# Kernel optimization log

Measured on AMD Instinct MI355X. Metric: run time of the kernel, lower is better.

## Reference

```python
import jax, jax.numpy as jnp
import numpy as np

HEADS = 4
DIM_HEAD = 128
HIDDEN = HEADS * DIM_HEAD  # 512
DIM = 256
EMBED = 256


def mish(x):
    return x * jnp.tanh(jax.nn.softplus(x))


def setup_inputs() -> dict:
    key = jax.random.key(0)
    k = jax.random.split(key, 7)
    b, a, f, t = 64, 8, DIM, 256
    x = jax.random.normal(k[0], (b, a, f, t), dtype=jnp.float32)
    time = jax.random.normal(k[1], (b, a, EMBED), dtype=jnp.float32)
    # to_qkv: Conv2d(dim, 3*hidden, 1, bias=False) -> weight [3*hidden, dim]
    w_qkv = jax.random.normal(k[2], (3 * HIDDEN, DIM), dtype=jnp.float32) * (1.0 / np.sqrt(DIM))
    # time_mlp: Mish -> Linear(embed, 3*hidden)
    w_time = jax.random.normal(k[3], (3 * HIDDEN, EMBED), dtype=jnp.float32) * (1.0 / np.sqrt(EMBED))
    b_time = jax.random.normal(k[4], (3 * HIDDEN,), dtype=jnp.float32) * 0.01
    # to_out: Conv2d(hidden, dim, 1) with bias
    w_out = jax.random.normal(k[5], (DIM, HIDDEN), dtype=jnp.float32) * (1.0 / np.sqrt(HIDDEN))
    b_out = jax.random.normal(k[6], (DIM,), dtype=jnp.float32) * 0.01
    return {"x": x, "time": time, "w_qkv": w_qkv, "w_time": w_time,
            "b_time": b_time, "w_out": w_out, "b_out": b_out}


def reference(x, time, w_qkv, w_time, b_time, w_out, b_out):
    b, a, f, t = x.shape
    heads, c = HEADS, DIM_HEAD
    # x: b a f t -> b f a t (channels-first for 1x1 conv)
    xp = jnp.transpose(x, (0, 2, 1, 3))  # [b, f, a, t]
    # 1x1 conv == channel GEMM
    qkv = jnp.einsum('of,bfat->boat', w_qkv, xp)  # [b, 3*hidden, a, t]
    # time MLP: Mish -> Linear; bias broadcast over t
    temb = mish(time) @ w_time.T + b_time          # [b, a, 3*hidden]
    temb = jnp.transpose(temb, (0, 2, 1))[..., None]  # [b, 3*hidden, a, 1]
    qkv = qkv + temb
    # 'b (qkv heads c) h w -> qkv (b h) heads c w' with h=a, w=t
    qkv = qkv.reshape(b, 3, heads, c, a, t)
    qkv = jnp.transpose(qkv, (1, 0, 4, 2, 3, 5)).reshape(3, b * a, heads, c, t)
    q, k, v = qkv[0], qkv[1], qkv[2]  # each [(b a), heads, c, t]
    k = jax.nn.softmax(k, axis=-1)
    # linear attention: context over keys/values, then apply to q
    context = jnp.einsum('bhdn,bhen->bhde', k, v)   # [(b a), heads, c, c]
    out = jnp.einsum('bhde,bhdn->bhen', context, q)  # [(b a), heads, c, t]
    # '(b h) heads c w -> b (heads c) h w'
    out = out.reshape(b, a, heads * c, t)
    out = jnp.transpose(out, (0, 2, 1, 3))  # [b, hidden, a, t]
    out = jnp.einsum('of,bfat->boat', w_out, out) + b_out[None, :, None, None]
    # b f a t -> b a f t
    return jnp.transpose(out, (0, 2, 1, 3))
```

## Files before the change

### kernel.cpp

```cpp
#include <hip/hip_runtime.h>

typedef __bf16 bf16;
typedef __bf16 bf16x4 __attribute__((ext_vector_type(4)));
typedef __bf16 bf16x8 __attribute__((ext_vector_type(8)));
typedef float  f32x4  __attribute__((ext_vector_type(4)));

#define TT    256
#define FF    256
#define NS    512

#define TSTR  40
#define TSZ2  (128 * TSTR)

#define SCHED0 __builtin_amdgcn_sched_barrier(0)
#define BAR    __builtin_amdgcn_s_barrier()
#define WAITVM(N) asm volatile("s_waitcnt vmcnt(" #N ")" ::: "memory")
#define WAITLGKM0 asm volatile("s_waitcnt lgkmcnt(0)" ::: "memory")

static __device__ inline f32x4 mfma16(bf16x8 a, bf16x8 b, f32x4 c) {
    return __builtin_amdgcn_mfma_f32_16x16x32_bf16(a, b, c, 0, 0, 0);
}

typedef const __attribute__((address_space(1))) unsigned int* gp_t;
typedef __attribute__((address_space(3))) unsigned int* lp_t;
static __device__ inline void gll16(const bf16* g, bf16* l) {
    __builtin_amdgcn_global_load_lds((gp_t)g, (lp_t)l, 16, 0, 0);
}


static __device__ inline void stage128g(const bf16* __restrict__ g, int ld, bf16* __restrict__ l) {
    int lane = threadIdx.x & 63, wv = threadIdx.x >> 6;
    int r = lane >> 2;
    int c8 = ((lane & 3) ^ ((lane >> 3) & 3)) * 8;
#pragma unroll
    for (int i = 0; i < 2; i++) {
        int row0 = wv * 32 + i * 16;
        gll16(g + (size_t)(row0 + r) * ld + c8, l + row0 * 32);
    }
}
static __device__ inline void stage8(const bf16* __restrict__ g, int ld, bf16* __restrict__ l) {
    int lane = threadIdx.x & 63, wv = threadIdx.x >> 6;
    int r = lane >> 2;
    int c8 = ((lane & 3) ^ ((lane >> 3) & 3)) * 8;
    int row0 = wv * 16;
    gll16(g + (size_t)(row0 + r) * ld + c8, l + row0 * 32);
}
static __device__ inline bf16x8 fragld(const bf16* __restrict__ l, int row0) {
    int lane = threadIdx.x & 63;
    int r15 = lane & 15;
    int kg = (lane >> 4) ^ ((r15 >> 1) & 3);
    return *(const bf16x8*)(l + (row0 + r15) * 32 + kg * 8);
}
static __device__ inline bf16x8 fragld_s(const bf16* __restrict__ l, int row0, int stride) {
    int lane = threadIdx.x & 63;
    return *(const bf16x8*)(l + (row0 + (lane & 15)) * stride + (lane >> 4) * 8);
}

__global__ __launch_bounds__(256) void k_cvt(const float4* __restrict__ src, bf16* __restrict__ dst) {
    int i = blockIdx.x * 256 + threadIdx.x;
    float4 v = src[i];
    bf16x4 o;
    o[0] = (__bf16)v.x; o[1] = (__bf16)v.y; o[2] = (__bf16)v.z; o[3] = (__bf16)v.w;
    *(bf16x4*)(dst + (size_t)i * 4) = o;
}

__global__ __launch_bounds__(256) void k_mish(const float4* __restrict__ src, bf16* __restrict__ dst) {
    int i = blockIdx.x * 256 + threadIdx.x;
    float4 v = src[i];
    float in[4] = {v.x, v.y, v.z, v.w};
    bf16x4 o;
#pragma unroll
    for (int j = 0; j < 4; j++) {
        float sp = log1pf(__expf(in[j]));
        o[j] = (__bf16)(in[j] * tanhf(sp));
    }
    *(bf16x4*)(dst + (size_t)i * 4) = o;
}

__global__ __launch_bounds__(256) void k_xpose(const float* __restrict__ x, bf16* __restrict__ xT) {
    __shared__ float tile[64][65];
    int bid = blockIdx.x;
    int s  = bid >> 4;
    int f0 = ((bid >> 2) & 3) * 64;
    int t0 = (bid & 3) * 64;
    int tid = threadIdx.x;
    int rr = tid >> 4;
    int cc = (tid & 15) * 4;
    const float* xp = x + ((size_t)(s * FF + f0)) * TT + t0;
#pragma unroll
    for (int i = 0; i < 4; i++) {
        int r = i * 16 + rr;
        float4 v = *(const float4*)(xp + (size_t)r * TT + cc);
        tile[r][cc] = v.x; tile[r][cc + 1] = v.y; tile[r][cc + 2] = v.z; tile[r][cc + 3] = v.w;
    }
    __syncthreads();
    bf16* op = xT + ((size_t)(s * TT + t0)) * FF + f0;
#pragma unroll
    for (int i = 0; i < 4; i++) {
        int tr = i * 16 + rr;
        bf16x4 o;
        o[0] = (__bf16)tile[cc][tr];     o[1] = (__bf16)tile[cc + 1][tr];
        o[2] = (__bf16)tile[cc + 2][tr]; o[3] = (__bf16)tile[cc + 3][tr];
        *(bf16x4*)(op + (size_t)tr * FF + cc) = o;
    }
}

__global__ __launch_bounds__(256) void k_temb(const bf16* __restrict__ wt, const bf16* __restrict__ mish,
                                              const float* __restrict__ bt, float* __restrict__ tembT) {
    __shared__ bf16 lA[128 * 32];
    __shared__ bf16 lB[128 * 32];
    int o0 = blockIdx.x * 128, s0 = blockIdx.y * 128;
    int tid = threadIdx.x, wv = tid >> 6, lane = tid & 63, qd = lane >> 4, c = lane & 15;
    f32x4 acc[2][8] = {};
    for (int k0 = 0; k0 < 256; k0 += 32) {
        __syncthreads();
        stage128g(wt + (size_t)o0 * 256 + k0, 256, lA);
        stage128g(mish + (size_t)s0 * 256 + k0, 256, lB);
        __syncthreads();
        bf16x8 a0 = fragld(lA, wv * 32), a1 = fragld(lA, wv * 32 + 16);
#pragma unroll
        for (int nt = 0; nt < 8; nt++) {
            bf16x8 b = fragld(lB, nt * 16);
            acc[0][nt] = mfma16(a0, b, acc[0][nt]);
            acc[1][nt] = mfma16(a1, b, acc[1][nt]);
        }
    }
#pragma unroll
    for (int mt = 0; mt < 2; mt++)
#pragma unroll
        for (int nt = 0; nt < 8; nt++)
#pragma unroll
            for (int r = 0; r < 4; r++) {
                int o = o0 + wv * 32 + mt * 16 + qd * 4 + r;
                int s = s0 + nt * 16 + c;
                tembT[(size_t)o * 512 + s] = acc[mt][nt][r] + bt[o];
            }
}

#define LXF(i)  ((bf16*)(smem + (size_t)(i) * 8192))
#define LWAF(i) ((bf16*)(smem + 24576 + (size_t)(i) * 8192))
#define LWBF(i) ((bf16*)(smem + 49152 + (size_t)(i) * 8192))
__global__ __launch_bounds__(512) void k_fused(const bf16* __restrict__ wqkv, const bf16* __restrict__ xT,
                                               const float* __restrict__ tembT, bf16* __restrict__ midT) {
    __shared__ __align__(16) char smem[156160];
    float* ls  = (float*)(smem + 73728);
    bf16*  lk  = (bf16*)(smem + 74240);
    bf16*  lct = (bf16*)(smem + 74240);
    bf16*  lv  = (bf16*)(smem + 115200);
    bf16*  lq  = (bf16*)(smem + 115200);

    int b = blockIdx.x;
    int w = (b & 7) * (4 * NS / 8) + (b >> 3);
    int s = w >> 2, h = w & 3;
    int tid = threadIdx.x, wv = tid >> 6, lane = tid & 63, qd = lane >> 4, c = lane & 15;
    const bf16* xs = xT + (size_t)s * (TT * FF);
    const bf16* Wq = wqkv + (size_t)(h * 128) * 256;
    const bf16* Wk = wqkv + (size_t)(512 + h * 128) * 256;
    const bf16* Wv = wqkv + (size_t)(1024 + h * 128) * 256;

    if (tid < 128) ls[tid] = 0.f;

    f32x4 cacc[8] = {};

    float tbk[8], tbv[8];
#pragma unroll
    for (int nt = 0; nt < 8; nt++) {
        tbk[nt] = tembT[(size_t)(512 + h * 128 + nt * 16 + c) * 512 + s];
        tbv[nt] = tembT[(size_t)(1024 + h * 128 + nt * 16 + c) * 512 + s];
    }

    for (int th = 0; th < 2; th++) {
        f32x4 kacc[8] = {}, vacc[8] = {};
        const bf16* xh = xs + (size_t)th * 128 * 256;
        stage8(xh,      256, LXF(0)); stage8(Wk,      256, LWAF(0)); stage8(Wv,      256, LWBF(0)); SCHED0;
        stage8(xh + 32, 256, LXF(1)); stage8(Wk + 32, 256, LWAF(1)); stage8(Wv + 32, 256, LWBF(1)); SCHED0;
        stage8(xh + 64, 256, LXF(2)); stage8(Wk + 64, 256, LWAF(2)); stage8(Wv + 64, 256, LWBF(2)); SCHED0;
#pragma unroll
        for (int t = 0; t < 8; t++) {
            if (t == 7)      { WAITVM(0); }
            else if (t == 6) { WAITVM(3); }
            else             { WAITVM(6); }
            SCHED0; BAR; SCHED0;
            int tb = t % 3;
            bf16x8 a0 = fragld(LXF(tb), wv * 16);
#pragma unroll
            for (int nt = 0; nt < 8; nt++) {
                kacc[nt] = mfma16(a0, fragld(LWAF(tb), nt * 16), kacc[nt]);
                vacc[nt] = mfma16(a0, fragld(LWBF(tb), nt * 16), vacc[nt]);
            }
            SCHED0; BAR; SCHED0;
            if (t + 3 < 8) {
                stage8(xh + (t + 3) * 32, 256, LXF(tb));
                stage8(Wk + (t + 3) * 32, 256, LWAF(tb));
                stage8(Wv + (t + 3) * 32, 256, LWBF(tb));
            }
            SCHED0;
        }
        {
            int addr0 = (wv >> 1) * TSZ2 + (wv & 1) * 16 + qd * 4;
#pragma unroll
            for (int nt = 0; nt < 8; nt++) {
                bf16x4 ok, ov;
                float ps = 0.f;
#pragma unroll
                for (int r = 0; r < 4; r++) {
                    bf16 e = (__bf16)__expf(kacc[nt][r] + tbk[nt]);
                    ok[r] = e; ps += (float)e;
                    ov[r] = (__bf16)(vacc[nt][r] + tbv[nt]);
                }
                int ad = addr0 + (nt * 16 + c) * TSTR;
                *(bf16x4*)(lk + ad) = ok;
                *(bf16x4*)(lv + ad) = ov;
                ps += __shfl_xor(ps, 16);
                ps += __shfl_xor(ps, 32);
                if (qd == 0) atomicAdd(&ls[nt * 16 + c], ps);
            }
        }
        __syncthreads();
#pragma unroll
        for (int tc = 0; tc < 4; tc++) {
            bf16x8 a0 = fragld_s(lv + tc * TSZ2, wv * 16, TSTR);
#pragma unroll
            for (int nt = 0; nt < 8; nt++)
                cacc[nt] = mfma16(a0, fragld_s(lk + tc * TSZ2, nt * 16, TSTR), cacc[nt]);
        }
        __syncthreads();
    }

    stage8(xs,      256, LXF(0)); stage8(Wq,      256, LWAF(0)); SCHED0;
    stage8(xs + 32, 256, LXF(1)); stage8(Wq + 32, 256, LWAF(1)); SCHED0;
    stage8(xs + 64, 256, LXF(2)); stage8(Wq + 64, 256, LWAF(2)); SCHED0;

#pragma unroll
    for (int nt = 0; nt < 8; nt++) {
        int d = nt * 16 + c;
        float rv = 1.0f / ls[d];
#pragma unroll
        for (int r = 0; r < 4; r++)
            lct[(wv * 16 + qd * 4 + r) * 136 + d] = (__bf16)(cacc[nt][r] * rv);
    }
    WAITLGKM0;
    SCHED0; BAR; SCHED0;

    float tbq[4];
#pragma unroll
    for (int r = 0; r < 4; r++)
        tbq[r] = tembT[(size_t)(h * 128 + wv * 16 + qd * 4 + r) * 512 + s];
    for (int th = 0; th < 2; th++) {
        f32x4 qacc[8] = {};
        const bf16* xh = xs + (size_t)th * 128 * 256;
        if (th == 1) {
            stage8(xh,      256, LXF(0)); stage8(Wq,      256, LWAF(0)); SCHED0;
            stage8(xh + 32, 256, LXF(1)); stage8(Wq + 32, 256, LWAF(1)); SCHED0;
            stage8(xh + 64, 256, LXF(2)); stage8(Wq + 64, 256, LWAF(2)); SCHED0;
        }
#pragma unroll
        for (int t = 0; t < 8; t++) {
            if (t == 7)      { WAITVM(0); }
            else if (t == 6) { WAITVM(2); }
            else             { WAITVM(4); }
            SCHED0; BAR; SCHED0;
            int tb = t % 3;
            bf16x8 a0 = fragld(LWAF(tb), wv * 16);
#pragma unroll
            for (int nt = 0; nt < 8; nt++)
                qacc[nt] = mfma16(a0, fragld(LXF(tb), nt * 16), qacc[nt]);
            SCHED0; BAR; SCHED0;
            if (t + 3 < 8) {
                stage8(xh + (t + 3) * 32, 256, LXF(tb));
                stage8(Wq + (t + 3) * 32, 256, LWAF(tb));
            }
            SCHED0;
        }
        {
            int addr0 = (wv >> 1) * TSZ2 + (wv & 1) * 16 + qd * 4;
#pragma unroll
            for (int nt = 0; nt < 8; nt++) {
                bf16x4 oq;
#pragma unroll
                for (int r = 0; r < 4; r++) oq[r] = (__bf16)(qacc[nt][r] + tbq[r]);
                *(bf16x4*)(lq + addr0 + (nt * 16 + c) * TSTR) = oq;
            }
        }
        __syncthreads();
        f32x4 oacc[8] = {};
#pragma unroll
        for (int dd = 0; dd < 4; dd++) {
            bf16x8 a0 = fragld_s(lct + dd * 32, wv * 16, 136);
#pragma unroll
            for (int nt = 0; nt < 8; nt++)
                oacc[nt] = mfma16(a0, fragld_s(lq + dd * TSZ2, nt * 16, TSTR), oacc[nt]);
        }
#pragma unroll
        for (int nt = 0; nt < 8; nt++) {
            int t = th * 128 + nt * 16 + c;
            int e = wv * 16 + qd * 4;
            bf16x4 o;
#pragma unroll
            for (int r = 0; r < 4; r++) o[r] = (__bf16)oacc[nt][r];
            *(bf16x4*)(midT + ((size_t)s * 256 + t) * 512 + h * 128 + e) = o;
        }
        __syncthreads();
    }
}

__global__ __launch_bounds__(256) void k_out(const bf16* __restrict__ wo, const bf16* __restrict__ midT,
                                             const float* __restrict__ bo, float* __restrict__ y) {
    __shared__ bf16 lA[2][128 * 32];
    __shared__ bf16 lB[2][128 * 32];
    int b = blockIdx.x;
    int w = (b & 7) * (4 * NS / 8) + (b >> 3);
    int s = w >> 2, j = w & 3;
    int o0 = (j >> 1) * 128, t0 = (j & 1) * 128;
    int tid = threadIdx.x, wv = tid >> 6, lane = tid & 63, qd = lane >> 4, c = lane & 15;
    const bf16* wA = wo + (size_t)o0 * 512;
    const bf16* ms = midT + (size_t)s * 131072 + (size_t)t0 * 512;
    f32x4 acc[2][8] = {};
    stage128g(wA, 512, lA[0]);
    stage128g(ms, 512, lB[0]);
    SCHED0;
    stage128g(wA + 32, 512, lA[1]);
    stage128g(ms + 32, 512, lB[1]);
    SCHED0;
#pragma unroll
    for (int t = 0; t < 16; t++) {
        if (t == 15) { WAITVM(0); } else { WAITVM(4); }
        SCHED0; BAR; SCHED0;
        bf16x8 a0 = fragld(lA[t & 1], wv * 32), a1 = fragld(lA[t & 1], wv * 32 + 16);
#pragma unroll
        for (int nt = 0; nt < 8; nt++) {
            bf16x8 bfr = fragld(lB[t & 1], nt * 16);
            acc[0][nt] = mfma16(a0, bfr, acc[0][nt]);
            acc[1][nt] = mfma16(a1, bfr, acc[1][nt]);
        }
        SCHED0; BAR; SCHED0;
        if (t + 2 < 16) {
            stage128g(wA + (t + 2) * 32, 512, lA[t & 1]);
            stage128g(ms + (t + 2) * 32, 512, lB[t & 1]);
        }
        SCHED0;
    }
    float bb[2][4];
#pragma unroll
    for (int mt = 0; mt < 2; mt++)
#pragma unroll
        for (int r = 0; r < 4; r++)
            bb[mt][r] = bo[o0 + wv * 32 + mt * 16 + qd * 4 + r];
#pragma unroll
    for (int mt = 0; mt < 2; mt++)
#pragma unroll
        for (int nt = 0; nt < 8; nt++)
#pragma unroll
            for (int r = 0; r < 4; r++) {
                int o = o0 + wv * 32 + mt * 16 + qd * 4 + r;
                int t = t0 + nt * 16 + c;
                y[((size_t)(s * 256 + o)) * 256 + t] = acc[mt][nt][r] + bb[mt][r];
            }
}

extern "C" void kernel_launch(void* const* d_in, const int* in_sizes, int n_in,
                              void* d_out, int out_size, void* d_ws, size_t ws_size,
                              hipStream_t stream) {
    const float* x      = (const float*)d_in[0];
    const float* time_  = (const float*)d_in[1];
    const float* w_qkv  = (const float*)d_in[2];
    const float* w_time = (const float*)d_in[3];
    const float* b_time = (const float*)d_in[4];
    const float* w_out  = (const float*)d_in[5];
    const float* b_out  = (const float*)d_in[6];
    float* y = (float*)d_out;
    char* ws = (char*)d_ws;

    bf16*  wqkv_bf  = (bf16*)(ws + 0);
    bf16*  wtime_bf = (bf16*)(ws + 786432);
    bf16*  wout_bf  = (bf16*)(ws + 1572864);
    bf16*  mish_bf  = (bf16*)(ws + 1835008);
    float* tembT    = (float*)(ws + 2097152);
    bf16*  xT       = (bf16*)(ws + 5242880);
    bf16*  midT     = (bf16*)(ws + 72351744);

    k_cvt<<<384, 256, 0, stream>>>((const float4*)w_qkv, wqkv_bf);
    k_cvt<<<384, 256, 0, stream>>>((const float4*)w_time, wtime_bf);
    k_cvt<<<128, 256, 0, stream>>>((const float4*)w_out, wout_bf);
    k_mish<<<128, 256, 0, stream>>>((const float4*)time_, mish_bf);
    k_temb<<<dim3(12, 4), 256, 0, stream>>>(wtime_bf, mish_bf, b_time, tembT);

    k_xpose<<<NS * 16, 256, 0, stream>>>(x, xT);
    k_fused<<<NS * 4, 512, 0, stream>>>(wqkv_bf, xT, tembT, midT);
    k_out<<<NS * 4, 256, 0, stream>>>(wout_bf, midT, b_out, y);
}
```

Baseline: 563.7 us.

## Retile fused kernel waves to 2x4 MFMA tiles and halve barriers

In the fused QKV/attention kernel, each wave now computes a 32x64 output tile instead of 16x128. Each A fragment feeds four MFMAs and each B fragment feeds two, which cuts LDS fragment reads. The K-loop now handles two K-steps per barrier pair, using the same three-buffer ring and adjusted vmcnt waits, and launch bounds add a min-blocks hint. The output GEMM kernel moves from double to triple buffering, also with two K-steps per barrier, at the cost of more LDS and register pressure.

Measured after the change: 552.7 us. No clear change (-2.0%).

```diff
diff --git a/kernel.cpp b/kernel.cpp
--- a/kernel.cpp
+++ b/kernel.cpp
@@ -140,8 +140,12 @@
 #define LXF(i)  ((bf16*)(smem + (size_t)(i) * 8192))
 #define LWAF(i) ((bf16*)(smem + 24576 + (size_t)(i) * 8192))
 #define LWBF(i) ((bf16*)(smem + 49152 + (size_t)(i) * 8192))
-__global__ __launch_bounds__(512) void k_fused(const bf16* __restrict__ wqkv, const bf16* __restrict__ xT,
-                                               const float* __restrict__ tembT, bf16* __restrict__ midT) {
+#define KV_STAGE(st) { int _b = (st) % 3; stage8(xh + (st) * 32, 256, LXF(_b)); \
+                       stage8(Wk + (st) * 32, 256, LWAF(_b)); stage8(Wv + (st) * 32, 256, LWBF(_b)); }
+#define Q_STAGE(st)  { int _b = (st) % 3; stage8(xh2 + (st) * 32, 256, LXF(_b)); \
+                       stage8(Wq + (st) * 32, 256, LWAF(_b)); }
+__global__ __launch_bounds__(512, 2) void k_fused(const bf16* __restrict__ wqkv, const bf16* __restrict__ xT,
+                                                  const float* __restrict__ tembT, bf16* __restrict__ midT) {
     __shared__ __align__(16) char smem[156160];
     float* ls  = (float*)(smem + 73728);
     bf16*  lk  = (bf16*)(smem + 74240);
@@ -153,6 +157,8 @@
     int w = (b & 7) * (4 * NS / 8) + (b >> 3);
     int s = w >> 2, h = w & 3;
     int tid = threadIdx.x, wv = tid >> 6, lane = tid & 63, qd = lane >> 4, c = lane & 15;
+    int wa = wv >> 1;
+    int wb = wv & 1;
     const bf16* xs = xT + (size_t)s * (TT * FF);
     const bf16* Wq = wqkv + (size_t)(h * 128) * 256;
     const bf16* Wk = wqkv + (size_t)(512 + h * 128) * 256;
@@ -160,154 +166,180 @@
 
     if (tid < 128) ls[tid] = 0.f;
 
-    f32x4 cacc[8] = {};
-
-    float tbk[8], tbv[8];
-#pragma unroll
-    for (int nt = 0; nt < 8; nt++) {
-        tbk[nt] = tembT[(size_t)(512 + h * 128 + nt * 16 + c) * 512 + s];
-        tbv[nt] = tembT[(size_t)(1024 + h * 128 + nt * 16 + c) * 512 + s];
+    f32x4 cacc[2][4] = {};
+
+    float tbk2[4], tbv2[4];
+#pragma unroll
+    for (int nt = 0; nt < 4; nt++) {
+        int ch = wb * 64 + nt * 16 + c;
+        tbk2[nt] = tembT[(size_t)(512 + h * 128 + ch) * 512 + s];
+        tbv2[nt] = tembT[(size_t)(1024 + h * 128 + ch) * 512 + s];
     }
 
     for (int th = 0; th < 2; th++) {
-        f32x4 kacc[8] = {}, vacc[8] = {};
+        f32x4 kacc[2][4] = {}, vacc[2][4] = {};
         const bf16* xh = xs + (size_t)th * 128 * 256;
-        stage8(xh,      256, LXF(0)); stage8(Wk,      256, LWAF(0)); stage8(Wv,      256, LWBF(0)); SCHED0;
-        stage8(xh + 32, 256, LXF(1)); stage8(Wk + 32, 256, LWAF(1)); stage8(Wv + 32, 256, LWBF(1)); SCHED0;
-        stage8(xh + 64, 256, LXF(2)); stage8(Wk + 64, 256, LWAF(2)); stage8(Wv + 64, 256, LWBF(2)); SCHED0;
-#pragma unroll
-        for (int t = 0; t < 8; t++) {
-            if (t == 7)      { WAITVM(0); }
-            else if (t == 6) { WAITVM(3); }
-            else             { WAITVM(6); }
+        KV_STAGE(0); SCHED0; KV_STAGE(1); SCHED0; KV_STAGE(2); SCHED0;
+#pragma unroll
+        for (int p = 0; p < 4; p++) {
+            if (p == 3) { WAITVM(0); } else { WAITVM(3); }
             SCHED0; BAR; SCHED0;
-            int tb = t % 3;
-            bf16x8 a0 = fragld(LXF(tb), wv * 16);
-#pragma unroll
-            for (int nt = 0; nt < 8; nt++) {
-                kacc[nt] = mfma16(a0, fragld(LWAF(tb), nt * 16), kacc[nt]);
-                vacc[nt] = mfma16(a0, fragld(LWBF(tb), nt * 16), vacc[nt]);
+#pragma unroll
+            for (int u = 0; u < 2; u++) {
+                int tb = (2 * p + u) % 3;
+                bf16x8 a0 = fragld(LXF(tb), wa * 32);
+                bf16x8 a1 = fragld(LXF(tb), wa * 32 + 16);
+#pragma unroll
+                for (int nt = 0; nt < 4; nt++) {
+                    int row = wb * 64 + nt * 16;
+                    bf16x8 bk = fragld(LWAF(tb), row);
+                    bf16x8 bv = fragld(LWBF(tb), row);
+                    kacc[0][nt] = mfma16(a0, bk, kacc[0][nt]);
+                    kacc[1][nt] = mfma16(a1, bk, kacc[1][nt]);
+                    vacc[0][nt] = mfma16(a0, bv, vacc[0][nt]);
+                    vacc[1][nt] = mfma16(a1, bv, vacc[1][nt]);
+                }
             }
             SCHED0; BAR; SCHED0;
-            if (t + 3 < 8) {
-                stage8(xh + (t + 3) * 32, 256, LXF(tb));
-                stage8(Wk + (t + 3) * 32, 256, LWAF(tb));
-                stage8(Wv + (t + 3) * 32, 256, LWBF(tb));
-            }
+            if (p == 0) { KV_STAGE(3); KV_STAGE(4); }
+            else if (p == 1) { KV_STAGE(5); KV_STAGE(6); }
+            else if (p == 2) { KV_STAGE(7); }
             SCHED0;
         }
         {
-            int addr0 = (wv >> 1) * TSZ2 + (wv & 1) * 16 + qd * 4;
-#pragma unroll
-            for (int nt = 0; nt < 8; nt++) {
-                bf16x4 ok, ov;
+#pragma unroll
+            for (int nt = 0; nt < 4; nt++) {
+                int ch = wb * 64 + nt * 16 + c;
                 float ps = 0.f;
+                bf16x4 ok0, ok1, ov0, ov1;
 #pragma unroll
                 for (int r = 0; r < 4; r++) {
-                    bf16 e = (__bf16)__expf(kacc[nt][r] + tbk[nt]);
-                    ok[r] = e; ps += (float)e;
-                    ov[r] = (__bf16)(vacc[nt][r] + tbv[nt]);
+                    bf16 e0 = (__bf16)__expf(kacc[0][nt][r] + tbk2[nt]);
+                    bf16 e1 = (__bf16)__expf(kacc[1][nt][r] + tbk2[nt]);
+                    ok0[r] = e0; ok1[r] = e1; ps += (float)e0 + (float)e1;
+                    ov0[r] = (__bf16)(vacc[0][nt][r] + tbv2[nt]);
+                    ov1[r] = (__bf16)(vacc[1][nt][r] + tbv2[nt]);
                 }
-                int ad = addr0 + (nt * 16 + c) * TSTR;
-                *(bf16x4*)(lk + ad) = ok;
-                *(bf16x4*)(lv + ad) = ov;
+                int ad = wa * TSZ2 + ch * TSTR + qd * 4;
+                *(bf16x4*)(lk + ad)      = ok0;
+                *(bf16x4*)(lk + ad + 16) = ok1;
+                *(bf16x4*)(lv + ad)      = ov0;
+                *(bf16x4*)(lv + ad + 16) = ov1;
                 ps += __shfl_xor(ps, 16);
                 ps += __shfl_xor(ps, 32);
-                if (qd == 0) atomicAdd(&ls[nt * 16 + c], ps);
+                if (qd == 0) atomicAdd(&ls[ch], ps);
             }
         }
         __syncthreads();
 #pragma unroll
         for (int tc = 0; tc < 4; tc++) {
-            bf16x8 a0 = fragld_s(lv + tc * TSZ2, wv * 16, TSTR);
-#pragma unroll
-            for (int nt = 0; nt < 8; nt++)
-                cacc[nt] = mfma16(a0, fragld_s(lk + tc * TSZ2, nt * 16, TSTR), cacc[nt]);
-        }
-        __syncthreads();
-    }
-
-    stage8(xs,      256, LXF(0)); stage8(Wq,      256, LWAF(0)); SCHED0;
-    stage8(xs + 32, 256, LXF(1)); stage8(Wq + 32, 256, LWAF(1)); SCHED0;
-    stage8(xs + 64, 256, LXF(2)); stage8(Wq + 64, 256, LWAF(2)); SCHED0;
-
-#pragma unroll
-    for (int nt = 0; nt < 8; nt++) {
-        int d = nt * 16 + c;
-        float rv = 1.0f / ls[d];
-#pragma unroll
-        for (int r = 0; r < 4; r++)
-            lct[(wv * 16 + qd * 4 + r) * 136 + d] = (__bf16)(cacc[nt][r] * rv);
-    }
+            bf16x8 a0 = fragld_s(lv + tc * TSZ2, wa * 32, TSTR);
+            bf16x8 a1 = fragld_s(lv + tc * TSZ2, wa * 32 + 16, TSTR);
+#pragma unroll
+            for (int nt = 0; nt < 4; nt++) {
+                bf16x8 kf = fragld_s(lk + tc * TSZ2, wb * 64 + nt * 16, TSTR);
+                cacc[0][nt] = mfma16(a0, kf, cacc[0][nt]);
+                cacc[1][nt] = mfma16(a1, kf, cacc[1][nt]);
+            }
+        }
+        __syncthreads();
+    }
+
+    {
+        const bf16* xh2 = xs;
+        Q_STAGE(0); SCHED0; Q_STAGE(1); SCHED0; Q_STAGE(2); SCHED0;
+    }
+
+#pragma unroll
+    for (int ai = 0; ai < 2; ai++)
+#pragma unroll
+        for (int nt = 0; nt < 4; nt++) {
+            int d = wb * 64 + nt * 16 + c;
+            float rv = 1.0f / ls[d];
+#pragma unroll
+            for (int r = 0; r < 4; r++)
+                lct[(wa * 32 + ai * 16 + qd * 4 + r) * 136 + d] = (__bf16)(cacc[ai][nt][r] * rv);
+        }
     WAITLGKM0;
     SCHED0; BAR; SCHED0;
 
-    float tbq[4];
-#pragma unroll
-    for (int r = 0; r < 4; r++)
-        tbq[r] = tembT[(size_t)(h * 128 + wv * 16 + qd * 4 + r) * 512 + s];
+    float tbq2[2][4];
+#pragma unroll
+    for (int ai = 0; ai < 2; ai++)
+#pragma unroll
+        for (int r = 0; r < 4; r++)
+            tbq2[ai][r] = tembT[(size_t)(h * 128 + wa * 32 + ai * 16 + qd * 4 + r) * 512 + s];
     for (int th = 0; th < 2; th++) {
-        f32x4 qacc[8] = {};
-        const bf16* xh = xs + (size_t)th * 128 * 256;
-        if (th == 1) {
-            stage8(xh,      256, LXF(0)); stage8(Wq,      256, LWAF(0)); SCHED0;
-            stage8(xh + 32, 256, LXF(1)); stage8(Wq + 32, 256, LWAF(1)); SCHED0;
-            stage8(xh + 64, 256, LXF(2)); stage8(Wq + 64, 256, LWAF(2)); SCHED0;
-        }
-#pragma unroll
-        for (int t = 0; t < 8; t++) {
-            if (t == 7)      { WAITVM(0); }
-            else if (t == 6) { WAITVM(2); }
-            else             { WAITVM(4); }
+        f32x4 qacc[2][4] = {};
+        const bf16* xh2 = xs + (size_t)th * 128 * 256;
+        if (th == 1) { Q_STAGE(0); SCHED0; Q_STAGE(1); SCHED0; Q_STAGE(2); SCHED0; }
+#pragma unroll
+        for (int p = 0; p < 4; p++) {
+            if (p == 3) { WAITVM(0); } else { WAITVM(2); }
             SCHED0; BAR; SCHED0;
-            int tb = t % 3;
-            bf16x8 a0 = fragld(LWAF(tb), wv * 16);
-#pragma unroll
-            for (int nt = 0; nt < 8; nt++)
-                qacc[nt] = mfma16(a0, fragld(LXF(tb), nt * 16), qacc[nt]);
+#pragma unroll
+            for (int u = 0; u < 2; u++) {
+                int tb = (2 * p + u) % 3;
+                bf16x8 a0 = fragld(LWAF(tb), wa * 32);
+                bf16x8 a1 = fragld(LWAF(tb), wa * 32 + 16);
+#pragma unroll
+                for (int nt = 0; nt < 4; nt++) {
+                    bf16x8 xf = fragld(LXF(tb), wb * 64 + nt * 16);
+                    qacc[0][nt] = mfma16(a0, xf, qacc[0][nt]);
+                    qacc[1][nt] = mfma16(a1, xf, qacc[1][nt]);
+                }
+            }
             SCHED0; BAR; SCHED0;
-            if (t + 3 < 8) {
-                stage8(xh + (t + 3) * 32, 256, LXF(tb));
-                stage8(Wq + (t + 3) * 32, 256, LWAF(tb));
-            }
+            if (p == 0) { Q_STAGE(3); Q_STAGE(4); }
+            else if (p == 1) { Q_STAGE(5); Q_STAGE(6); }
+            else if (p == 2) { Q_STAGE(7); }
             SCHED0;
         }
         {
-            int addr0 = (wv >> 1) * TSZ2 + (wv & 1) * 16 + qd * 4;
-#pragma unroll
-            for (int nt = 0; nt < 8; nt++) {
-                bf16x4 oq;
-#pragma unroll
-                for (int r = 0; r < 4; r++) oq[r] = (__bf16)(qacc[nt][r] + tbq[r]);
-                *(bf16x4*)(lq + addr0 + (nt * 16 + c) * TSTR) = oq;
-            }
-        }
-        __syncthreads();
-        f32x4 oacc[8] = {};
+#pragma unroll
+            for (int nt = 0; nt < 4; nt++) {
+                int t = wb * 64 + nt * 16 + c;
+#pragma unroll
+                for (int ai = 0; ai < 2; ai++) {
+                    bf16x4 oq;
+#pragma unroll
+                    for (int r = 0; r < 4; r++) oq[r] = (__bf16)(qacc[ai][nt][r] + tbq2[ai][r]);
+                    *(bf16x4*)(lq + wa * TSZ2 + t * TSTR + ai * 16 + qd * 4) = oq;
+                }
+            }
+        }
+        __syncthreads();
+        f32x4 oacc[2][4] = {};
 #pragma unroll
         for (int dd = 0; dd < 4; dd++) {
-            bf16x8 a0 = fragld_s(lct + dd * 32, wv * 16, 136);
-#pragma unroll
-            for (int nt = 0; nt < 8; nt++)
-                oacc[nt] = mfma16(a0, fragld_s(lq + dd * TSZ2, nt * 16, TSTR), oacc[nt]);
-        }
-#pragma unroll
-        for (int nt = 0; nt < 8; nt++) {
-            int t = th * 128 + nt * 16 + c;
-            int e = wv * 16 + qd * 4;
-            bf16x4 o;
-#pragma unroll
-            for (int r = 0; r < 4; r++) o[r] = (__bf16)oacc[nt][r];
-            *(bf16x4*)(midT + ((size_t)s * 256 + t) * 512 + h * 128 + e) = o;
-        }
+            bf16x8 a0 = fragld_s(lct + dd * 32, wa * 32, 136);
+            bf16x8 a1 = fragld_s(lct + dd * 32, wa * 32 + 16, 136);
+#pragma unroll
+            for (int nt = 0; nt < 4; nt++) {
+                bf16x8 qf = fragld_s(lq + dd * TSZ2, wb * 64 + nt * 16, TSTR);
+                oacc[0][nt] = mfma16(a0, qf, oacc[0][nt]);
+                oacc[1][nt] = mfma16(a1, qf, oacc[1][nt]);
+            }
+        }
+#pragma unroll
+        for (int nt = 0; nt < 4; nt++)
+#pragma unroll
+            for (int ai = 0; ai < 2; ai++) {
+                int t = th * 128 + wb * 64 + nt * 16 + c;
+                int e = wa * 32 + ai * 16 + qd * 4;
+                bf16x4 o;
+#pragma unroll
+                for (int r = 0; r < 4; r++) o[r] = (__bf16)oacc[ai][nt][r];
+                *(bf16x4*)(midT + ((size_t)s * 256 + t) * 512 + h * 128 + e) = o;
+            }
         __syncthreads();
     }
 }
 
 __global__ __launch_bounds__(256) void k_out(const bf16* __restrict__ wo, const bf16* __restrict__ midT,
                                              const float* __restrict__ bo, float* __restrict__ y) {
-    __shared__ bf16 lA[2][128 * 32];
-    __shared__ bf16 lB[2][128 * 32];
+    __shared__ bf16 lA[3][128 * 32];
+    __shared__ bf16 lB[3][128 * 32];
     int b = blockIdx.x;
     int w = (b & 7) * (4 * NS / 8) + (b >> 3);
     int s = w >> 2, j = w & 3;
@@ -316,27 +348,31 @@
     const bf16* wA = wo + (size_t)o0 * 512;
     const bf16* ms = midT + (size_t)s * 131072 + (size_t)t0 * 512;
     f32x4 acc[2][8] = {};
-    stage128g(wA, 512, lA[0]);
-    stage128g(ms, 512, lB[0]);
-    SCHED0;
-    stage128g(wA + 32, 512, lA[1]);
-    stage128g(ms + 32, 512, lB[1]);
-    SCHED0;
-#pragma unroll
-    for (int t = 0; t < 16; t++) {
-        if (t == 15) { WAITVM(0); } else { WAITVM(4); }
+    stage128g(wA, 512, lA[0]);       stage128g(ms, 512, lB[0]);       SCHED0;
+    stage128g(wA + 32, 512, lA[1]);  stage128g(ms + 32, 512, lB[1]);  SCHED0;
+    stage128g(wA + 64, 512, lA[2]);  stage128g(ms + 64, 512, lB[2]);  SCHED0;
+#pragma unroll
+    for (int p = 0; p < 8; p++) {
+        if (p == 7) { WAITVM(0); } else { WAITVM(4); }
         SCHED0; BAR; SCHED0;
-        bf16x8 a0 = fragld(lA[t & 1], wv * 32), a1 = fragld(lA[t & 1], wv * 32 + 16);
-#pragma unroll
-        for (int nt = 0; nt < 8; nt++) {
-            bf16x8 bfr = fragld(lB[t & 1], nt * 16);
-            acc[0][nt] = mfma16(a0, bfr, acc[0][nt]);
-            acc[1][nt] = mfma16(a1, bfr, acc[1][nt]);
+#pragma unroll
+        for (int u = 0; u < 2; u++) {
+            int tb = (2 * p + u) % 3;
+            bf16x8 a0 = fragld(lA[tb], wv * 32), a1 = fragld(lA[tb], wv * 32 + 16);
+#pragma unroll
+            for (int nt = 0; nt < 8; nt++) {
+                bf16x8 bfr = fragld(lB[tb], nt * 16);
+                acc[0][nt] = mfma16(a0, bfr, acc[0][nt]);
+                acc[1][nt] = mfma16(a1, bfr, acc[1][nt]);
+            }
         }
         SCHED0; BAR; SCHED0;
-        if (t + 2 < 16) {
-            stage128g(wA + (t + 2) * 32, 512, lA[t & 1]);
-            stage128g(ms + (t + 2) * 32, 512, lB[t & 1]);
+        {
+            int s1 = 2 * p + 3;
+            if (s1 < 16)     { stage128g(wA + s1 * 32, 512, lA[s1 % 3]);
+                               stage128g(ms + s1 * 32, 512, lB[s1 % 3]); }
+            if (s1 + 1 < 16) { stage128g(wA + (s1 + 1) * 32, 512, lA[(s1 + 1) % 3]);
+                               stage128g(ms + (s1 + 1) * 32, 512, lB[(s1 + 1) % 3]); }
         }
         SCHED0;
     }
```
